# Kernel tuning notes

Measured on AMD Instinct MI355X. Metric: run time of the kernel, lower is better.

The kernel has to match this reference:

```python
import jax, jax.numpy as jnp
import numpy as np

B, L, HS, WS = 4, 5, 32, 32
C = 256            # dim == heads * dim_head
M, D = 8, 32       # heads, dim_head
T, R = 2, 4        # num_types, num_relations
I = M * D          # inner_dim
EPS = 1e-5


def setup_inputs() -> dict:
    key = jax.random.key(0)
    ks = jax.random.split(key, 12)
    w = 0.02
    x = jax.random.normal(ks[0], (B, L, HS, WS, C), dtype=jnp.float32)
    mask = jnp.ones((B, HS, WS, L, L), dtype=jnp.int32)
    prior_encoding = jax.random.randint(ks[1], (B, L, HS, WS, 3), 0, T).astype(jnp.float32)
    return {
        "x": x,
        "mask": mask,
        "prior_encoding": prior_encoding,
        "ln_w": jnp.ones((C,), jnp.float32),
        "ln_b": jnp.zeros((C,), jnp.float32),
        "Wq": jax.random.normal(ks[2], (T, C, I), jnp.float32) * w,
        "bq": jnp.zeros((T, I), jnp.float32),
        "Wk": jax.random.normal(ks[3], (T, C, I), jnp.float32) * w,
        "bk": jnp.zeros((T, I), jnp.float32),
        "Wv": jax.random.normal(ks[4], (T, C, I), jnp.float32) * w,
        "bv": jnp.zeros((T, I), jnp.float32),
        "Wa": jax.random.normal(ks[5], (T, I, C), jnp.float32) * w,
        "ba": jnp.zeros((T, C), jnp.float32),
        "rel_att": jax.random.normal(ks[6], (R, M, D, D), jnp.float32) * w,
        "rel_msg": jax.random.normal(ks[7], (R, M, D, D), jnp.float32) * w,
    }


def _hgt_forward(x, mask, prior_encoding, ln_w, ln_b, Wq, bq, Wk, bk, Wv, bv, Wa, ba, rel_att, rel_msg):
    # pre-LayerNorm over channel dim
    mu = jnp.mean(x, axis=-1, keepdims=True)
    var = jnp.mean(jnp.square(x - mu), axis=-1, keepdims=True)
    xn = (x - mu) * jax.lax.rsqrt(var + EPS) * ln_w + ln_b

    # [B,L,H,W,C] -> [B,H,W,L,C]
    xp = jnp.transpose(xn, (0, 2, 3, 1, 4))
    types = prior_encoding[:, :, 0, 0, 2].astype(jnp.int32)  # [B,L]

    # per-type q/k/v projections via gather of type-indexed weights
    q = jnp.einsum('bhwlc,blci->bhwli', xp, Wq[types]) + bq[types][:, None, None]
    k = jnp.einsum('bhwlc,blci->bhwli', xp, Wk[types]) + bk[types][:, None, None]
    v = jnp.einsum('bhwlc,blci->bhwli', xp, Wv[types]) + bv[types][:, None, None]

    def to_heads(t):  # [B,H,W,L,I] -> [B,M,H,W,L,D]
        return jnp.transpose(t.reshape(B, HS, WS, L, M, D), (0, 4, 1, 2, 3, 5))
    q, k, v = to_heads(q), to_heads(k), to_heads(v)

    # relation-indexed edge weights: e_type = t_i * T + t_j
    e = types[:, :, None] * T + types[:, None, :]              # [B,L,L]
    w_att = jnp.transpose(rel_att[e], (0, 3, 1, 2, 4, 5))      # [B,M,L,L,D,D]
    w_msg = jnp.transpose(rel_msg[e], (0, 3, 1, 2, 4, 5))

    scale = D ** -0.5
    q_w = jnp.einsum('bmhwip,bmijpq->bmhwijq', q, w_att)
    att = jnp.einsum('bmhwijq,bmhwjq->bmhwij', q_w, k) * scale
    att = jnp.where(mask[:, None] == 0, -1e9, att)
    att = jax.nn.softmax(att, axis=-1)

    v_msg = jnp.einsum('bmijpc,bmhwjp->bmhwijc', w_msg, v)
    out = jnp.einsum('bmhwij,bmhwijc->bmhwic', att, v_msg)

    # [B,M,H,W,L,D] -> [B,H,W,L,C]
    out = jnp.transpose(out, (0, 2, 3, 4, 1, 5)).reshape(B, HS, WS, L, I)
    out = jnp.einsum('bhwli,blic->bhwlc', out, Wa[types]) + ba[types][:, None, None]
    # dropout is identity at inference
    return jnp.transpose(out, (0, 3, 1, 2, 4))                 # [B,L,H,W,C]


def reference(x, mask, prior_encoding, ln_w, ln_b, Wq, bq, Wk, bk, Wv, bv, Wa, ba, rel_att, rel_msg):
    return _hgt_forward(x, mask, prior_encoding, ln_w, ln_b, Wq, bq, Wk, bk, Wv, bv, Wa, ba, rel_att, rel_msg)
```

## Files before the change

kernel.cpp:

```cpp
#include <hip/hip_runtime.h>
#include <hip/hip_bf16.h>
#include <math.h>

#define BB 4
#define LL 5
#define HSZ 32
#define WSZ 32
#define PP (HSZ*WSZ)
#define CC 256
#define MM 8
#define DD 32
#define II 256
#define TT 2
#define NTOK (BB*PP*LL*II)
#define TILE_ELEMS 8192
#define SCALE 0.17677669529663687f

typedef short bf16x8 __attribute__((ext_vector_type(8)));
typedef float f32x4 __attribute__((ext_vector_type(4)));

static __device__ __forceinline__ ushort f2bf(float f) {
    unsigned u = __float_as_uint(f);
    unsigned r = (u + 0x7fffu + ((u >> 16) & 1u)) >> 16;
    return (ushort)r;
}
static __device__ __forceinline__ float bf2f(ushort u) {
    return __uint_as_float(((unsigned)u) << 16);
}

__global__ __launch_bounds__(256) void k_combine(
    const float* __restrict__ Wq, const float* __restrict__ Wv,
    const float* __restrict__ Wk, const float* __restrict__ Wa,
    const float* __restrict__ bq, const float* __restrict__ bv,
    const float* __restrict__ rel_att, const float* __restrict__ rel_msg,
    ushort* __restrict__ packW, float* __restrict__ bEff)
{
    __shared__ float As[1024];
    const int blk = blockIdx.x;
    const int tid = threadIdx.x;
    if (blk < 64) {
        const int p  = blk >> 5;
        const int t  = (blk >> 4) & 1;
        const int ts = (blk >> 3) & 1;
        const int m  = blk & 7;
        const float* A = (p == 0)
            ? rel_att + (size_t)((t * 2 + ts) * 8 + m) * 1024
            : rel_msg + (size_t)((ts * 2 + t) * 8 + m) * 1024;
        for (int i = tid; i < 1024; i += 256) As[i] = A[i];
        __syncthreads();

        const float* W = ((p == 0) ? Wq : Wv) + (size_t)t * 65536;
        const int k = tid;
        float wrow[32];
        #pragma unroll
        for (int u = 0; u < 8; ++u)
            *(float4*)&wrow[u * 4] = *(const float4*)&W[k * 256 + m * 32 + u * 4];

        const int slot = (p == 0 ? 0 : 4) + t * 2 + ts;
        ushort* base = packW + (size_t)slot * 65536;
        const int kt = k >> 5, j = k & 7, lq = ((k >> 3) & 3) * 16;
        #pragma unroll
        for (int q = 0; q < 32; ++q) {
            float acc = 0.f;
            #pragma unroll
            for (int pp = 0; pp < 32; ++pp) acc += wrow[pp] * As[pp * 32 + q];
            const int nt = m * 2 + (q >> 4);
            const int lane = lq + (q & 15);
            base[(size_t)((nt * 8 + kt) * 64 + lane) * 8 + j] = f2bf(acc);
        }
        if (tid < 32) {
            const int q = tid;
            const float* bi = ((p == 0) ? bq : bv) + t * 256 + m * 32;
            float acc = 0.f;
            #pragma unroll
            for (int pp = 0; pp < 32; ++pp) acc += bi[pp] * As[pp * 32 + q];
            bEff[(p ? 1024 : 0) + (t * 2 + ts) * 256 + m * 32 + q] = acc;
        }
    } else {
        const int idx = blk - 64;
        const int which = idx >> 6;
        const int gi = (idx & 63) * 256 + tid;
        const int t = gi >> 13;
        const int sub = gi & 8191;
        const float* src = ((which == 0) ? Wk : Wa) + (size_t)t * 65536;
        const int slot = (which == 0 ? 8 : 10) + t;
        const int nt = sub >> 9, kt = (sub >> 6) & 7, lane = sub & 63;
        const int k0 = kt * 32 + (lane >> 4) * 8;
        const int n  = nt * 16 + (lane & 15);
        ushort h[8];
        #pragma unroll
        for (int j = 0; j < 8; ++j) h[j] = f2bf(src[(size_t)(k0 + j) * 256 + n]);
        uint4 o;
        o.x = (unsigned)h[0] | ((unsigned)h[1] << 16);
        o.y = (unsigned)h[2] | ((unsigned)h[3] << 16);
        o.z = (unsigned)h[4] | ((unsigned)h[5] << 16);
        o.w = (unsigned)h[6] | ((unsigned)h[7] << 16);
        *(uint4*)(packW + (size_t)slot * 65536 + (size_t)sub * 8) = o;
    }
}

__global__ __launch_bounds__(256) void k_ln(
    const float* __restrict__ x,
    const float* __restrict__ lnw, const float* __restrict__ lnb,
    ushort* __restrict__ xnPack)
{
    __shared__ ushort Apack[8192];

    const int tid = threadIdx.x;
    const int bl  = blockIdx.x >> 5;
    const int pt  = blockIdx.x & 31;
    const int p0  = pt * 32;

    const int r  = tid >> 3;
    const int jj = tid & 7;
    const float* xrow = x + ((size_t)bl * PP + p0 + r) * CC;
    float4 xv[8];
    float s1 = 0.f, s2 = 0.f;
    #pragma unroll
    for (int u = 0; u < 8; ++u) {
        xv[u] = *(const float4*)(xrow + jj * 32 + u * 4);
        s1 += xv[u].x + xv[u].y + xv[u].z + xv[u].w;
        s2 += xv[u].x * xv[u].x + xv[u].y * xv[u].y + xv[u].z * xv[u].z + xv[u].w * xv[u].w;
    }
    s1 += __shfl_xor(s1, 1); s1 += __shfl_xor(s1, 2); s1 += __shfl_xor(s1, 4);
    s2 += __shfl_xor(s2, 1); s2 += __shfl_xor(s2, 2); s2 += __shfl_xor(s2, 4);
    const float mu   = s1 * (1.0f / 256.0f);
    const float var  = s2 * (1.0f / 256.0f) - mu * mu;
    const float rstd = rsqrtf(var + 1e-5f);

    const int mt_r = r >> 4, rm = r & 15;
    #pragma unroll
    for (int u = 0; u < 8; ++u) {
        const int c0 = jj * 32 + u * 4;
        const float4 g  = *(const float4*)(lnw + c0);
        const float4 bt = *(const float4*)(lnb + c0);
        const ushort h0 = f2bf((xv[u].x - mu) * rstd * g.x + bt.x);
        const ushort h1 = f2bf((xv[u].y - mu) * rstd * g.y + bt.y);
        const ushort h2 = f2bf((xv[u].z - mu) * rstd * g.z + bt.z);
        const ushort h3 = f2bf((xv[u].w - mu) * rstd * g.w + bt.w);
        uint2 w2;
        w2.x = (unsigned)h0 | ((unsigned)h1 << 16);
        w2.y = (unsigned)h2 | ((unsigned)h3 << 16);
        const int kt   = c0 >> 5;
        const int lsub = rm + (((c0 >> 3) & 3) << 4);
        const int j0   = c0 & 7;
        *(uint2*)&Apack[(((mt_r * 8 + kt) * 64 + lsub) << 3) + j0] = w2;
    }
    __syncthreads();

    const size_t tbase = (size_t)blockIdx.x * TILE_ELEMS;
    #pragma unroll
    for (int u = 0; u < 4; ++u) {
        const int ch = (tid + u * 256) * 8;
        *(uint4*)&xnPack[tbase + ch] = *(const uint4*)&Apack[ch];
    }
}

__global__ __launch_bounds__(256) void k_proj(
    const ushort* __restrict__ xnPack, const float* __restrict__ prior,
    const ushort* __restrict__ packW, const float* __restrict__ bEff,
    const float* __restrict__ bk,
    ushort* __restrict__ qw0, ushort* __restrict__ qw1, ushort* __restrict__ kkO,
    ushort* __restrict__ vm0, ushort* __restrict__ vm1)
{
    __shared__ ushort As[8192];

    const int tid  = threadIdx.x;
    const int blk  = blockIdx.x;
    const int mat  = blk / 320;
    const int rem  = blk - mat * 320;
    const int bl   = rem >> 4;
    const int sub  = rem & 15;
    const int pg   = sub >> 1;
    const int half = sub & 1;
    const int bbi  = bl / LL;
    const int l    = bl - bbi * LL;
    const int t    = (int)prior[(size_t)bl * (PP * 3) + 2];

    int slot; const float* bias;
    if (mat < 2)       { slot = t * 2 + mat;           bias = bEff + slot * 256; }
    else if (mat == 2) { slot = 8 + t;                 bias = bk + t * 256; }
    else               { slot = 4 + t * 2 + (mat - 3); bias = bEff + 1024 + (t * 2 + (mat - 3)) * 256; }
    ushort* dst = (mat == 0) ? qw0 : (mat == 1) ? qw1 : (mat == 2) ? kkO : (mat == 3) ? vm0 : vm1;

    const int wv = tid >> 6, lane = tid & 63;

    const ushort* Bp = packW + (size_t)slot * 65536;
    bf16x8 bfr[8][2];
    #pragma unroll
    for (int kt = 0; kt < 8; ++kt)
        #pragma unroll
        for (int nn = 0; nn < 2; ++nn) {
            const int ntg = half * 8 + wv * 2 + nn;
            bfr[kt][nn] = *(const bf16x8*)&Bp[(size_t)((ntg * 8 + kt) * 64 + lane) * 8];
        }

    const int cl = lane & 15, rq = lane >> 4;
    const int colA = half * 128 + wv * 32 + cl;
    const int colB = colA + 16;
    const float biasA = bias[colA], biasB = bias[colB];

    #pragma unroll 1
    for (int tl = 0; tl < 4; ++tl) {
        const int pt = pg * 4 + tl;
        const size_t tbase = (size_t)(bl * 32 + pt) * TILE_ELEMS;
        __syncthreads();
        #pragma unroll
        for (int u = 0; u < 4; ++u) {
            const int ch = (tid + u * 256) * 8;
            *(uint4*)&As[ch] = *(const uint4*)&xnPack[tbase + ch];
        }
        __syncthreads();

        f32x4 acc[2][2];
        #pragma unroll
        for (int mt = 0; mt < 2; ++mt)
            #pragma unroll
            for (int nn = 0; nn < 2; ++nn)
                acc[mt][nn] = (f32x4){0.f, 0.f, 0.f, 0.f};

        #pragma unroll
        for (int kt = 0; kt < 8; ++kt) {
            const bf16x8 a0 = *(const bf16x8*)&As[((0 * 8 + kt) * 64 + lane) << 3];
            const bf16x8 a1 = *(const bf16x8*)&As[((1 * 8 + kt) * 64 + lane) << 3];
            acc[0][0] = __builtin_amdgcn_mfma_f32_16x16x32_bf16(a0, bfr[kt][0], acc[0][0], 0, 0, 0);
            acc[0][1] = __builtin_amdgcn_mfma_f32_16x16x32_bf16(a0, bfr[kt][1], acc[0][1], 0, 0, 0);
            acc[1][0] = __builtin_amdgcn_mfma_f32_16x16x32_bf16(a1, bfr[kt][0], acc[1][0], 0, 0, 0);
            acc[1][1] = __builtin_amdgcn_mfma_f32_16x16x32_bf16(a1, bfr[kt][1], acc[1][1], 0, 0, 0);
        }

        const int p0 = pt * 32;
        #pragma unroll
        for (int mt = 0; mt < 2; ++mt) {
            const int row0 = p0 + mt * 16 + rq * 4;
            #pragma unroll
            for (int r2 = 0; r2 < 4; ++r2) {
                const size_t rb = ((size_t)(bbi * PP + row0 + r2) * LL + l) * II;
                dst[rb + colA] = f2bf(acc[mt][0][r2] + biasA);
                dst[rb + colB] = f2bf(acc[mt][1][r2] + biasB);
            }
        }
    }
}

__global__ __launch_bounds__(256) void k_attn_lite(
    const ushort* __restrict__ qw0, const ushort* __restrict__ qw1,
    const ushort* __restrict__ kkI,
    const ushort* __restrict__ vm0, const ushort* __restrict__ vm1,
    const int* __restrict__ mask, const float* __restrict__ prior,
    ushort* __restrict__ aoPack)
{
    const int tid  = threadIdx.x;
    const int site = blockIdx.x * 4 + (tid >> 6);
    const int lane = tid & 63;
    const int b    = site >> 10;
    const int pix  = site & 1023;
    const int c0   = lane * 4;

    int ty[5];
    #pragma unroll
    for (int l = 0; l < 5; ++l)
        ty[l] = (int)prior[(size_t)(b * 5 + l) * (PP * 3) + 2];

    float qf[2][5][4], kf[5][4], vf[2][5][4];
    #pragma unroll
    for (int l = 0; l < 5; ++l) {
        const size_t base = ((size_t)site * 5 + l) * II + c0;
        const ushort4 q0 = *(const ushort4*)(qw0 + base);
        const ushort4 q1 = *(const ushort4*)(qw1 + base);
        const ushort4 kv = *(const ushort4*)(kkI + base);
        const ushort4 v0 = *(const ushort4*)(vm0 + base);
        const ushort4 v1 = *(const ushort4*)(vm1 + base);
        qf[0][l][0] = bf2f(q0.x); qf[0][l][1] = bf2f(q0.y); qf[0][l][2] = bf2f(q0.z); qf[0][l][3] = bf2f(q0.w);
        qf[1][l][0] = bf2f(q1.x); qf[1][l][1] = bf2f(q1.y); qf[1][l][2] = bf2f(q1.z); qf[1][l][3] = bf2f(q1.w);
        kf[l][0]    = bf2f(kv.x); kf[l][1]    = bf2f(kv.y); kf[l][2]    = bf2f(kv.z); kf[l][3]    = bf2f(kv.w);
        vf[0][l][0] = bf2f(v0.x); vf[0][l][1] = bf2f(v0.y); vf[0][l][2] = bf2f(v0.z); vf[0][l][3] = bf2f(v0.w);
        vf[1][l][0] = bf2f(v1.x); vf[1][l][1] = bf2f(v1.y); vf[1][l][2] = bf2f(v1.z); vf[1][l][3] = bf2f(v1.w);
    }

    const int rr   = pix & 31;
    const int tile0 = b * 5 * 32 + (pix >> 5);
    const int mt   = rr >> 4;
    const int ktc  = c0 >> 5;
    const int lp   = (rr & 15) + 16 * ((c0 >> 3) & 3);
    const int j0   = c0 & 7;
    const int fofs = ((mt * 8 + ktc) * 64 + lp) * 8 + j0;

    #pragma unroll
    for (int i = 0; i < 5; ++i) {
        float lg[5];
        #pragma unroll
        for (int j = 0; j < 5; ++j) {
            const float s0 = qf[0][i][0] * kf[j][0] + qf[0][i][1] * kf[j][1]
                           + qf[0][i][2] * kf[j][2] + qf[0][i][3] * kf[j][3];
            const float s1 = qf[1][i][0] * kf[j][0] + qf[1][i][1] * kf[j][1]
                           + qf[1][i][2] * kf[j][2] + qf[1][i][3] * kf[j][3];
            float s = ty[j] ? s1 : s0;
            s += __shfl_xor(s, 1); s += __shfl_xor(s, 2); s += __shfl_xor(s, 4);
            const int mv = mask[((size_t)site * 5 + i) * 5 + j];
            lg[j] = mv ? s * SCALE : -1e9f;
        }
        float mx = lg[0];
        #pragma unroll
        for (int j = 1; j < 5; ++j) mx = fmaxf(mx, lg[j]);
        float ex[5], sum = 0.f;
        #pragma unroll
        for (int j = 0; j < 5; ++j) { ex[j] = __expf(lg[j] - mx); sum += ex[j]; }
        const float rs = 1.0f / sum;
        float o0 = 0.f, o1 = 0.f, o2 = 0.f, o3 = 0.f;
        #pragma unroll
        for (int j = 0; j < 5; ++j) {
            const float w = ex[j] * rs;
            o0 += w * (ty[i] ? vf[1][j][0] : vf[0][j][0]);
            o1 += w * (ty[i] ? vf[1][j][1] : vf[0][j][1]);
            o2 += w * (ty[i] ? vf[1][j][2] : vf[0][j][2]);
            o3 += w * (ty[i] ? vf[1][j][3] : vf[0][j][3]);
        }
        uint2 w2;
        w2.x = (unsigned)f2bf(o0) | ((unsigned)f2bf(o1) << 16);
        w2.y = (unsigned)f2bf(o2) | ((unsigned)f2bf(o3) << 16);
        *(uint2*)&aoPack[(size_t)(tile0 + i * 32) * TILE_ELEMS + fofs] = w2;
    }
}

__global__ __launch_bounds__(256) void k_out(
    const ushort* __restrict__ aoPack, const float* __restrict__ prior,
    const ushort* __restrict__ packW, const float* __restrict__ ba,
    float* __restrict__ out)
{
    __shared__ ushort As[8192];

    const int tid  = threadIdx.x;
    const int blk  = blockIdx.x;
    const int bl   = blk >> 5;
    const int sub  = blk & 31;
    const int pg   = sub >> 1;
    const int half = sub & 1;
    const int bbi  = bl / LL;
    const int l    = bl - bbi * LL;
    const int t    = (int)prior[(size_t)bl * (PP * 3) + 2];

    const int wv = tid >> 6, lane = tid & 63;
    const ushort* Bp = packW + (size_t)(10 + t) * 65536;
    bf16x8 bfr[8][2];
    #pragma unroll
    for (int kt = 0; kt < 8; ++kt)
        #pragma unroll
        for (int nn = 0; nn < 2; ++nn) {
            const int ntg = half * 8 + wv * 2 + nn;
            bfr[kt][nn] = *(const bf16x8*)&Bp[(size_t)((ntg * 8 + kt) * 64 + lane) * 8];
        }

    const int cl = lane & 15, rq = lane >> 4;
    const int colA = half * 128 + wv * 32 + cl;
    const int colB = colA + 16;
    const float biasA = ba[t * CC + colA], biasB = ba[t * CC + colB];

    #pragma unroll 1
    for (int tl = 0; tl < 2; ++tl) {
        const int pt = pg * 2 + tl;
        const size_t tbase = (size_t)(bl * 32 + pt) * TILE_ELEMS;
        __syncthreads();
        #pragma unroll
        for (int u = 0; u < 4; ++u) {
            const int ch = (tid + u * 256) * 8;
            *(uint4*)&As[ch] = *(const uint4*)&aoPack[tbase + ch];
        }
        __syncthreads();

        f32x4 acc[2][2];
        #pragma unroll
        for (int mt = 0; mt < 2; ++mt)
            #pragma unroll
            for (int nn = 0; nn < 2; ++nn)
                acc[mt][nn] = (f32x4){0.f, 0.f, 0.f, 0.f};

        #pragma unroll
        for (int kt = 0; kt < 8; ++kt) {
            const bf16x8 a0 = *(const bf16x8*)&As[((0 * 8 + kt) * 64 + lane) << 3];
            const bf16x8 a1 = *(const bf16x8*)&As[((1 * 8 + kt) * 64 + lane) << 3];
            acc[0][0] = __builtin_amdgcn_mfma_f32_16x16x32_bf16(a0, bfr[kt][0], acc[0][0], 0, 0, 0);
            acc[0][1] = __builtin_amdgcn_mfma_f32_16x16x32_bf16(a0, bfr[kt][1], acc[0][1], 0, 0, 0);
            acc[1][0] = __builtin_amdgcn_mfma_f32_16x16x32_bf16(a1, bfr[kt][0], acc[1][0], 0, 0, 0);
            acc[1][1] = __builtin_amdgcn_mfma_f32_16x16x32_bf16(a1, bfr[kt][1], acc[1][1], 0, 0, 0);
        }

        const int p0 = pt * 32;
        #pragma unroll
        for (int mt = 0; mt < 2; ++mt) {
            const int row0 = p0 + mt * 16 + rq * 4;
            #pragma unroll
            for (int r2 = 0; r2 < 4; ++r2) {
                float* rb = out + ((size_t)(bbi * LL + l) * PP + row0 + r2) * CC;
                rb[colA] = acc[mt][0][r2] + biasA;
                rb[colB] = acc[mt][1][r2] + biasB;
            }
        }
    }
}

extern "C" void kernel_launch(void* const* d_in, const int* in_sizes, int n_in,
                              void* d_out, int out_size, void* d_ws, size_t ws_size,
                              hipStream_t stream) {
    const float* x       = (const float*)d_in[0];
    const int*   mask    = (const int*)d_in[1];
    const float* prior   = (const float*)d_in[2];
    const float* lnw     = (const float*)d_in[3];
    const float* lnb     = (const float*)d_in[4];
    const float* Wq      = (const float*)d_in[5];
    const float* bq      = (const float*)d_in[6];
    const float* Wk      = (const float*)d_in[7];
    const float* bk      = (const float*)d_in[8];
    const float* Wv      = (const float*)d_in[9];
    const float* bv      = (const float*)d_in[10];
    const float* Wa      = (const float*)d_in[11];
    const float* ba      = (const float*)d_in[12];
    const float* rel_att = (const float*)d_in[13];
    const float* rel_msg = (const float*)d_in[14];
    float* out = (float*)d_out;

    ushort* qw0    = (ushort*)d_ws;
    ushort* qw1    = qw0 + NTOK;
    ushort* kko    = qw1 + NTOK;
    ushort* vm0    = kko + NTOK;
    ushort* vm1    = vm0 + NTOK;
    ushort* aoPack = vm1 + NTOK;
    ushort* xnPack = aoPack + NTOK;
    ushort* packW  = xnPack + NTOK;
    float*  bEff   = (float*)(packW + 12 * 65536);

    hipLaunchKernelGGL(k_combine, dim3(192), dim3(256), 0, stream,
                       Wq, Wv, Wk, Wa, bq, bv, rel_att, rel_msg, packW, bEff);
    hipLaunchKernelGGL(k_ln, dim3(640), dim3(256), 0, stream,
                       x, lnw, lnb, xnPack);
    hipLaunchKernelGGL(k_proj, dim3(1600), dim3(256), 0, stream,
                       xnPack, prior, packW, bEff, bk, qw0, qw1, kko, vm0, vm1);
    hipLaunchKernelGGL(k_attn_lite, dim3(1024), dim3(256), 0, stream,
                       qw0, qw1, kko, vm0, vm1, mask, prior, aoPack);
    hipLaunchKernelGGL(k_out, dim3(640), dim3(256), 0, stream,
                       aoPack, prior, packW, ba, out);
}
```

Baseline: 154.4 us.

## Fuse weight-fold and LayerNorm kernels, regrid projections, stage output stores via LDS

Merges the weight-combination kernel and the LayerNorm kernel into one launch, with the block index deciding which job a block does. This removes one launch and lets the two independent jobs overlap. k_proj now gets twice as many blocks, each doing fewer tiles, and writes intermediates in [b,l,pix] order; the attention kernel's load indexing is updated to match. k_out gives one tile per block and stages results in shared memory so the fp32 output is written with coalesced float4 stores. The trade-off is more LDS per block and extra reloads of the B fragments across blocks.

Result: faster. 150.1 us, median of 2 (-2.8%).

```diff
diff --git a/kernel.cpp b/kernel.cpp
--- a/kernel.cpp
+++ b/kernel.cpp
@@ -28,16 +28,21 @@
     return __uint_as_float(((unsigned)u) << 16);
 }
 
-__global__ __launch_bounds__(256) void k_combine(
+__global__ __launch_bounds__(256) void k_fold(
     const float* __restrict__ Wq, const float* __restrict__ Wv,
     const float* __restrict__ Wk, const float* __restrict__ Wa,
     const float* __restrict__ bq, const float* __restrict__ bv,
     const float* __restrict__ rel_att, const float* __restrict__ rel_msg,
-    ushort* __restrict__ packW, float* __restrict__ bEff)
+    const float* __restrict__ x,
+    const float* __restrict__ lnw, const float* __restrict__ lnb,
+    ushort* __restrict__ packW, float* __restrict__ bEff,
+    ushort* __restrict__ xnPack)
 {
     __shared__ float As[1024];
+    __shared__ ushort Apack[8192];
     const int blk = blockIdx.x;
     const int tid = threadIdx.x;
+
     if (blk < 64) {
         const int p  = blk >> 5;
         const int t  = (blk >> 4) & 1;
@@ -76,7 +81,7 @@
             for (int pp = 0; pp < 32; ++pp) acc += bi[pp] * As[pp * 32 + q];
             bEff[(p ? 1024 : 0) + (t * 2 + ts) * 256 + m * 32 + q] = acc;
         }
-    } else {
+    } else if (blk < 192) {
         const int idx = blk - 64;
         const int which = idx >> 6;
         const int gi = (idx & 63) * 256 + tid;
@@ -96,63 +101,55 @@
         o.z = (unsigned)h[4] | ((unsigned)h[5] << 16);
         o.w = (unsigned)h[6] | ((unsigned)h[7] << 16);
         *(uint4*)(packW + (size_t)slot * 65536 + (size_t)sub * 8) = o;
-    }
-}
-
-__global__ __launch_bounds__(256) void k_ln(
-    const float* __restrict__ x,
-    const float* __restrict__ lnw, const float* __restrict__ lnb,
-    ushort* __restrict__ xnPack)
-{
-    __shared__ ushort Apack[8192];
-
-    const int tid = threadIdx.x;
-    const int bl  = blockIdx.x >> 5;
-    const int pt  = blockIdx.x & 31;
-    const int p0  = pt * 32;
-
-    const int r  = tid >> 3;
-    const int jj = tid & 7;
-    const float* xrow = x + ((size_t)bl * PP + p0 + r) * CC;
-    float4 xv[8];
-    float s1 = 0.f, s2 = 0.f;
-    #pragma unroll
-    for (int u = 0; u < 8; ++u) {
-        xv[u] = *(const float4*)(xrow + jj * 32 + u * 4);
-        s1 += xv[u].x + xv[u].y + xv[u].z + xv[u].w;
-        s2 += xv[u].x * xv[u].x + xv[u].y * xv[u].y + xv[u].z * xv[u].z + xv[u].w * xv[u].w;
-    }
-    s1 += __shfl_xor(s1, 1); s1 += __shfl_xor(s1, 2); s1 += __shfl_xor(s1, 4);
-    s2 += __shfl_xor(s2, 1); s2 += __shfl_xor(s2, 2); s2 += __shfl_xor(s2, 4);
-    const float mu   = s1 * (1.0f / 256.0f);
-    const float var  = s2 * (1.0f / 256.0f) - mu * mu;
-    const float rstd = rsqrtf(var + 1e-5f);
-
-    const int mt_r = r >> 4, rm = r & 15;
-    #pragma unroll
-    for (int u = 0; u < 8; ++u) {
-        const int c0 = jj * 32 + u * 4;
-        const float4 g  = *(const float4*)(lnw + c0);
-        const float4 bt = *(const float4*)(lnb + c0);
-        const ushort h0 = f2bf((xv[u].x - mu) * rstd * g.x + bt.x);
-        const ushort h1 = f2bf((xv[u].y - mu) * rstd * g.y + bt.y);
-        const ushort h2 = f2bf((xv[u].z - mu) * rstd * g.z + bt.z);
-        const ushort h3 = f2bf((xv[u].w - mu) * rstd * g.w + bt.w);
-        uint2 w2;
-        w2.x = (unsigned)h0 | ((unsigned)h1 << 16);
-        w2.y = (unsigned)h2 | ((unsigned)h3 << 16);
-        const int kt   = c0 >> 5;
-        const int lsub = rm + (((c0 >> 3) & 3) << 4);
-        const int j0   = c0 & 7;
-        *(uint2*)&Apack[(((mt_r * 8 + kt) * 64 + lsub) << 3) + j0] = w2;
-    }
-    __syncthreads();
-
-    const size_t tbase = (size_t)blockIdx.x * TILE_ELEMS;
-    #pragma unroll
-    for (int u = 0; u < 4; ++u) {
-        const int ch = (tid + u * 256) * 8;
-        *(uint4*)&xnPack[tbase + ch] = *(const uint4*)&Apack[ch];
+    } else {
+        const int lblk = blk - 192;
+        const int bl  = lblk >> 5;
+        const int pt  = lblk & 31;
+        const int p0  = pt * 32;
+
+        const int r  = tid >> 3;
+        const int jj = tid & 7;
+        const float* xrow = x + ((size_t)bl * PP + p0 + r) * CC;
+        float4 xv[8];
+        float s1 = 0.f, s2 = 0.f;
+        #pragma unroll
+        for (int u = 0; u < 8; ++u) {
+            xv[u] = *(const float4*)(xrow + jj * 32 + u * 4);
+            s1 += xv[u].x + xv[u].y + xv[u].z + xv[u].w;
+            s2 += xv[u].x * xv[u].x + xv[u].y * xv[u].y + xv[u].z * xv[u].z + xv[u].w * xv[u].w;
+        }
+        s1 += __shfl_xor(s1, 1); s1 += __shfl_xor(s1, 2); s1 += __shfl_xor(s1, 4);
+        s2 += __shfl_xor(s2, 1); s2 += __shfl_xor(s2, 2); s2 += __shfl_xor(s2, 4);
+        const float mu   = s1 * (1.0f / 256.0f);
+        const float var  = s2 * (1.0f / 256.0f) - mu * mu;
+        const float rstd = rsqrtf(var + 1e-5f);
+
+        const int mt_r = r >> 4, rm = r & 15;
+        #pragma unroll
+        for (int u = 0; u < 8; ++u) {
+            const int c0 = jj * 32 + u * 4;
+            const float4 g  = *(const float4*)(lnw + c0);
+            const float4 bt = *(const float4*)(lnb + c0);
+            const ushort h0 = f2bf((xv[u].x - mu) * rstd * g.x + bt.x);
+            const ushort h1 = f2bf((xv[u].y - mu) * rstd * g.y + bt.y);
+            const ushort h2 = f2bf((xv[u].z - mu) * rstd * g.z + bt.z);
+            const ushort h3 = f2bf((xv[u].w - mu) * rstd * g.w + bt.w);
+            uint2 w2;
+            w2.x = (unsigned)h0 | ((unsigned)h1 << 16);
+            w2.y = (unsigned)h2 | ((unsigned)h3 << 16);
+            const int kt   = c0 >> 5;
+            const int lsub = rm + (((c0 >> 3) & 3) << 4);
+            const int j0   = c0 & 7;
+            *(uint2*)&Apack[(((mt_r * 8 + kt) * 64 + lsub) << 3) + j0] = w2;
+        }
+        __syncthreads();
+
+        const size_t tbase = (size_t)lblk * TILE_ELEMS;
+        #pragma unroll
+        for (int u = 0; u < 4; ++u) {
+            const int ch = (tid + u * 256) * 8;
+            *(uint4*)&xnPack[tbase + ch] = *(const uint4*)&Apack[ch];
+        }
     }
 }
 
@@ -167,14 +164,12 @@
 
     const int tid  = threadIdx.x;
     const int blk  = blockIdx.x;
-    const int mat  = blk / 320;
-    const int rem  = blk - mat * 320;
-    const int bl   = rem >> 4;
-    const int sub  = rem & 15;
+    const int mat  = blk / 640;
+    const int rem  = blk - mat * 640;
+    const int bl   = rem >> 5;
+    const int sub  = rem & 31;
     const int pg   = sub >> 1;
     const int half = sub & 1;
-    const int bbi  = bl / LL;
-    const int l    = bl - bbi * LL;
     const int t    = (int)prior[(size_t)bl * (PP * 3) + 2];
 
     int slot; const float* bias;
@@ -201,8 +196,8 @@
     const float biasA = bias[colA], biasB = bias[colB];
 
     #pragma unroll 1
-    for (int tl = 0; tl < 4; ++tl) {
-        const int pt = pg * 4 + tl;
+    for (int tl = 0; tl < 2; ++tl) {
+        const int pt = pg * 2 + tl;
         const size_t tbase = (size_t)(bl * 32 + pt) * TILE_ELEMS;
         __syncthreads();
         #pragma unroll
@@ -235,7 +230,7 @@
             const int row0 = p0 + mt * 16 + rq * 4;
             #pragma unroll
             for (int r2 = 0; r2 < 4; ++r2) {
-                const size_t rb = ((size_t)(bbi * PP + row0 + r2) * LL + l) * II;
+                const size_t rb = ((size_t)bl * PP + row0 + r2) * II;
                 dst[rb + colA] = f2bf(acc[mt][0][r2] + biasA);
                 dst[rb + colB] = f2bf(acc[mt][1][r2] + biasB);
             }
@@ -265,7 +260,7 @@
     float qf[2][5][4], kf[5][4], vf[2][5][4];
     #pragma unroll
     for (int l = 0; l < 5; ++l) {
-        const size_t base = ((size_t)site * 5 + l) * II + c0;
+        const size_t base = (((size_t)(b * 5 + l) << 10) + pix) * II + c0;
         const ushort4 q0 = *(const ushort4*)(qw0 + base);
         const ushort4 q1 = *(const ushort4*)(qw1 + base);
         const ushort4 kv = *(const ushort4*)(kkI + base);
@@ -329,12 +324,13 @@
     float* __restrict__ out)
 {
     __shared__ ushort As[8192];
+    __shared__ float obufF[32 * 132];
 
     const int tid  = threadIdx.x;
     const int blk  = blockIdx.x;
-    const int bl   = blk >> 5;
-    const int sub  = blk & 31;
-    const int pg   = sub >> 1;
+    const int bl   = blk >> 6;
+    const int sub  = blk & 63;
+    const int pt   = sub >> 1;
     const int half = sub & 1;
     const int bbi  = bl / LL;
     const int l    = bl - bbi * LL;
@@ -351,51 +347,56 @@
             bfr[kt][nn] = *(const bf16x8*)&Bp[(size_t)((ntg * 8 + kt) * 64 + lane) * 8];
         }
 
+    const size_t tbase = (size_t)(bl * 32 + pt) * TILE_ELEMS;
+    #pragma unroll
+    for (int u = 0; u < 4; ++u) {
+        const int ch = (tid + u * 256) * 8;
+        *(uint4*)&As[ch] = *(const uint4*)&aoPack[tbase + ch];
+    }
+    __syncthreads();
+
     const int cl = lane & 15, rq = lane >> 4;
-    const int colA = half * 128 + wv * 32 + cl;
-    const int colB = colA + 16;
-    const float biasA = ba[t * CC + colA], biasB = ba[t * CC + colB];
-
-    #pragma unroll 1
-    for (int tl = 0; tl < 2; ++tl) {
-        const int pt = pg * 2 + tl;
-        const size_t tbase = (size_t)(bl * 32 + pt) * TILE_ELEMS;
-        __syncthreads();
-        #pragma unroll
-        for (int u = 0; u < 4; ++u) {
-            const int ch = (tid + u * 256) * 8;
-            *(uint4*)&As[ch] = *(const uint4*)&aoPack[tbase + ch];
-        }
-        __syncthreads();
-
-        f32x4 acc[2][2];
-        #pragma unroll
-        for (int mt = 0; mt < 2; ++mt)
-            #pragma unroll
-            for (int nn = 0; nn < 2; ++nn)
-                acc[mt][nn] = (f32x4){0.f, 0.f, 0.f, 0.f};
-
-        #pragma unroll
-        for (int kt = 0; kt < 8; ++kt) {
-            const bf16x8 a0 = *(const bf16x8*)&As[((0 * 8 + kt) * 64 + lane) << 3];
-            const bf16x8 a1 = *(const bf16x8*)&As[((1 * 8 + kt) * 64 + lane) << 3];
-            acc[0][0] = __builtin_amdgcn_mfma_f32_16x16x32_bf16(a0, bfr[kt][0], acc[0][0], 0, 0, 0);
-            acc[0][1] = __builtin_amdgcn_mfma_f32_16x16x32_bf16(a0, bfr[kt][1], acc[0][1], 0, 0, 0);
-            acc[1][0] = __builtin_amdgcn_mfma_f32_16x16x32_bf16(a1, bfr[kt][0], acc[1][0], 0, 0, 0);
-            acc[1][1] = __builtin_amdgcn_mfma_f32_16x16x32_bf16(a1, bfr[kt][1], acc[1][1], 0, 0, 0);
-        }
-
-        const int p0 = pt * 32;
-        #pragma unroll
-        for (int mt = 0; mt < 2; ++mt) {
-            const int row0 = p0 + mt * 16 + rq * 4;
-            #pragma unroll
-            for (int r2 = 0; r2 < 4; ++r2) {
-                float* rb = out + ((size_t)(bbi * LL + l) * PP + row0 + r2) * CC;
-                rb[colA] = acc[mt][0][r2] + biasA;
-                rb[colB] = acc[mt][1][r2] + biasB;
-            }
-        }
+    const int colL_A = wv * 32 + cl;
+    const int colL_B = colL_A + 16;
+    const float biasA = ba[t * CC + half * 128 + colL_A];
+    const float biasB = ba[t * CC + half * 128 + colL_B];
+
+    f32x4 acc[2][2];
+    #pragma unroll
+    for (int mt = 0; mt < 2; ++mt)
+        #pragma unroll
+        for (int nn = 0; nn < 2; ++nn)
+            acc[mt][nn] = (f32x4){0.f, 0.f, 0.f, 0.f};
+
+    #pragma unroll
+    for (int kt = 0; kt < 8; ++kt) {
+        const bf16x8 a0 = *(const bf16x8*)&As[((0 * 8 + kt) * 64 + lane) << 3];
+        const bf16x8 a1 = *(const bf16x8*)&As[((1 * 8 + kt) * 64 + lane) << 3];
+        acc[0][0] = __builtin_amdgcn_mfma_f32_16x16x32_bf16(a0, bfr[kt][0], acc[0][0], 0, 0, 0);
+        acc[0][1] = __builtin_amdgcn_mfma_f32_16x16x32_bf16(a0, bfr[kt][1], acc[0][1], 0, 0, 0);
+        acc[1][0] = __builtin_amdgcn_mfma_f32_16x16x32_bf16(a1, bfr[kt][0], acc[1][0], 0, 0, 0);
+        acc[1][1] = __builtin_amdgcn_mfma_f32_16x16x32_bf16(a1, bfr[kt][1], acc[1][1], 0, 0, 0);
+    }
+
+    #pragma unroll
+    for (int mt = 0; mt < 2; ++mt) {
+        const int rowb = mt * 16 + rq * 4;
+        #pragma unroll
+        for (int r2 = 0; r2 < 4; ++r2) {
+            obufF[(rowb + r2) * 132 + colL_A] = acc[mt][0][r2] + biasA;
+            obufF[(rowb + r2) * 132 + colL_B] = acc[mt][1][r2] + biasB;
+        }
+    }
+    __syncthreads();
+
+    const int p0 = pt * 32;
+    #pragma unroll
+    for (int k2 = 0; k2 < 4; ++k2) {
+        const int id  = tid + k2 * 256;
+        const int row = id >> 5;
+        const int ch  = (id & 31) * 4;
+        const float4 v4 = *(const float4*)&obufF[row * 132 + ch];
+        *(float4*)(out + ((size_t)(bbi * LL + l) * PP + p0 + row) * CC + half * 128 + ch) = v4;
     }
 }
 
@@ -429,14 +430,13 @@
     ushort* packW  = xnPack + NTOK;
     float*  bEff   = (float*)(packW + 12 * 65536);
 
-    hipLaunchKernelGGL(k_combine, dim3(192), dim3(256), 0, stream,
-                       Wq, Wv, Wk, Wa, bq, bv, rel_att, rel_msg, packW, bEff);
-    hipLaunchKernelGGL(k_ln, dim3(640), dim3(256), 0, stream,
-                       x, lnw, lnb, xnPack);
-    hipLaunchKernelGGL(k_proj, dim3(1600), dim3(256), 0, stream,
+    hipLaunchKernelGGL(k_fold, dim3(832), dim3(256), 0, stream,
+                       Wq, Wv, Wk, Wa, bq, bv, rel_att, rel_msg,
+                       x, lnw, lnb, packW, bEff, xnPack);
+    hipLaunchKernelGGL(k_proj, dim3(3200), dim3(256), 0, stream,
                        xnPack, prior, packW, bEff, bk, qw0, qw1, kko, vm0, vm1);
     hipLaunchKernelGGL(k_attn_lite, dim3(1024), dim3(256), 0, stream,
                        qw0, qw1, kko, vm0, vm1, mask, prior, aoPack);
-    hipLaunchKernelGGL(k_out, dim3(640), dim3(256), 0, stream,
+    hipLaunchKernelGGL(k_out, dim3(1280), dim3(256), 0, stream,
                        aoPack, prior, packW, ba, out);
 }
```
